# Performance work log

Measured on AMD Instinct MI355X. Metric: run time of the kernel, lower is better.

The kernel has to match this reference:

```python
import jax, jax.numpy as jnp
import numpy as np
import math

B, F, S, D, NH, L, DFF, M = 8, 48, 64, 512, 8, 4, 2048, 64
PERIOD = 30
NEG = -1e9
EPS = 1e-5

def _slopes(n):
    start = 2.0 ** (-2.0 ** -(math.log2(n) - 3))
    return np.array([start * (start ** i) for i in range(n)], dtype=np.float32)

def _biased_mask():  # (NH, F, F): causal mask + periodic ALiBi bias, alibi[i,j] = -((i-j)//period)
    i = np.arange(F)[:, None]; j = np.arange(F)[None, :]
    alibi = -((i - j) // PERIOD).astype(np.float32)
    return jnp.asarray(np.where(j <= i, _slopes(NH)[:, None, None] * alibi, NEG).astype(np.float32))

def _ppe():  # (F, D): periodic sinusoidal positional encoding (period 30)
    pos = np.arange(PERIOD, dtype=np.float32)[:, None]
    div = np.exp(np.arange(0, D, 2, dtype=np.float32) * (-math.log(10000.0) / D))
    pe = np.zeros((PERIOD, D), np.float32)
    pe[:, 0::2] = np.sin(pos * div)
    pe[:, 1::2] = np.cos(pos * div)
    return jnp.asarray(np.tile(pe, (F // PERIOD + 1, 1))[:F])

BIASED_MASK = _biased_mask()
PE = _ppe()
MEM_MASK = jnp.where(jnp.eye(F, dtype=bool), 0.0, NEG)  # enc_dec diagonal mask (frame i <-> content i)

def _ln(x, g, b):
    mu = x.mean(-1, keepdims=True)
    var = ((x - mu) ** 2).mean(-1, keepdims=True)
    return (x - mu) * jax.lax.rsqrt(var + EPS) * g + b

def _mha(q, k, v, in_w, in_b, out_w, out_b, nh, mask=None):
    Bq, Tq, d = q.shape
    Tk = k.shape[1]
    dh = d // nh
    wq, wk, wv = jnp.split(in_w, 3, axis=0)
    bq, bk, bv = jnp.split(in_b, 3, axis=0)
    qh = (q @ wq.T + bq).reshape(Bq, Tq, nh, dh).transpose(0, 2, 1, 3)
    kh = (k @ wk.T + bk).reshape(Bq, Tk, nh, dh).transpose(0, 2, 1, 3)
    vh = (v @ wv.T + bv).reshape(Bq, Tk, nh, dh).transpose(0, 2, 1, 3)
    s = jnp.einsum('bhqd,bhkd->bhqk', qh, kh) / jnp.sqrt(jnp.float32(dh))
    if mask is not None:
        s = s + mask
    o = jnp.einsum('bhqk,bhkd->bhqd', jax.nn.softmax(s, axis=-1), vh)
    return o.transpose(0, 2, 1, 3).reshape(Bq, Tq, d) @ out_w.T + out_b

def setup_inputs():
    key = jax.random.key(0)
    ks = iter(jax.random.split(key, 40))
    r = lambda *sh: jax.random.normal(next(ks), sh, jnp.float32) * 0.02
    return dict(
        content_code=jax.random.normal(next(ks), (B, F, D), jnp.float32),
        style_code=jax.random.normal(next(ks), (B, D), jnp.float32),
        style_hiddens=jax.random.normal(next(ks), (B, S, D), jnp.float32),
        init_state=jax.random.normal(next(ks), (B, M), jnp.float32),
        ca_in_w=r(3 * D, D), ca_in_b=r(3 * D), ca_out_w=r(D, D), ca_out_b=r(D),
        se_w=r(D, 2 * D), se_b=r(D),
        mm_w=r(D, M), mm_b=r(D),
        mmr_w=r(M, D), mmr_b=r(M),
        sa_in_w=r(L, 3 * D, D), sa_in_b=r(L, 3 * D), sa_out_w=r(L, D, D), sa_out_b=r(L, D),
        xa_in_w=r(L, 3 * D, D), xa_in_b=r(L, 3 * D), xa_out_w=r(L, D, D), xa_out_b=r(L, D),
        ff1_w=r(L, DFF, D), ff1_b=r(L, DFF), ff2_w=r(L, D, DFF), ff2_b=r(L, D),
        ln_g=jnp.ones((L, 3, D), jnp.float32), ln_b=jnp.zeros((L, 3, D), jnp.float32),
    )

def _forward(content_code, style_code, style_hiddens, init_state,
             ca_in_w, ca_in_b, ca_out_w, ca_out_b, se_w, se_b,
             mm_w, mm_b, mmr_w, mmr_b,
             sa_in_w, sa_in_b, sa_out_w, sa_out_b,
             xa_in_w, xa_in_b, xa_out_w, xa_out_b,
             ff1_w, ff1_b, ff2_w, ff2_b, ln_g, ln_b):
    style_emb_g = style_code[:, None, :]
    # 1-head cross-attn of each content frame against style hiddens; the torch code
    # computes this one query (frame) at a time, which is mathematically identical.
    sel = _mha(content_code, style_hiddens, style_hiddens,
               ca_in_w, ca_in_b, ca_out_w, ca_out_b, 1)  # (B, F, D)

    def emb_new(feat, i):  # style_emb_map(cat([feat, style_emb_l_i])) + global style
        return (jnp.concatenate([feat, sel[:, i:i + 1]], -1) @ se_w.T + se_b) + style_emb_g

    def decoder(x, mem):  # post-norm TransformerDecoder, relu FFN, eval (no dropout)
        T = x.shape[1]
        tgt = BIASED_MASK[None, :, :T, :T]
        mmask = MEM_MASK[:T][None, None]  # (1,1,T,F)
        for l in range(L):
            x = _ln(x + _mha(x, x, x, sa_in_w[l], sa_in_b[l], sa_out_w[l], sa_out_b[l], NH, tgt),
                    ln_g[l, 0], ln_b[l, 0])
            x = _ln(x + _mha(x, mem, mem, xa_in_w[l], xa_in_b[l], xa_out_w[l], xa_out_b[l], NH, mmask),
                    ln_g[l, 1], ln_b[l, 1])
            h = jax.nn.relu(x @ ff1_w[l].T + ff1_b[l]) @ ff2_w[l].T + ff2_b[l]
            x = _ln(x + h, ln_g[l, 2], ln_b[l, 2])
        return x

    dec_emb = emb_new((init_state @ mm_w.T + mm_b)[:, None], 0)  # (B,1,D)
    dec_out = None
    for i in range(F):
        dec_input = dec_emb + PE[:dec_emb.shape[1]]
        dec_out = decoder(dec_input, content_code) @ mmr_w.T + mmr_b  # (B, i+1, M)
        new = dec_out[:, -1:] @ mm_w.T + mm_b
        dec_emb = jnp.concatenate([dec_emb, emb_new(new, i)], axis=1)
    return dec_out, sel

def reference(content_code, style_code, style_hiddens, init_state,
              ca_in_w, ca_in_b, ca_out_w, ca_out_b, se_w, se_b,
              mm_w, mm_b, mmr_w, mmr_b,
              sa_in_w, sa_in_b, sa_out_w, sa_out_b,
              xa_in_w, xa_in_b, xa_out_w, xa_out_b,
              ff1_w, ff1_b, ff2_w, ff2_b, ln_g, ln_b):
    return _forward(content_code, style_code, style_hiddens, init_state,
                    ca_in_w, ca_in_b, ca_out_w, ca_out_b, se_w, se_b,
                    mm_w, mm_b, mmr_w, mmr_b,
                    sa_in_w, sa_in_b, sa_out_w, sa_out_b,
                    xa_in_w, xa_in_b, xa_out_w, xa_out_b,
                    ff1_w, ff1_b, ff2_w, ff2_b, ln_g, ln_b)
```

## Files before the change

### kernel.cpp

```cpp
#include <hip/hip_runtime.h>
#include <hip/hip_fp16.h>


typedef _Float16 h2 __attribute__((ext_vector_type(2)));
__device__ inline h2 u2h(unsigned u){ union{unsigned u; h2 h;} c; c.u=u; return c.h; }
#if __has_builtin(__builtin_amdgcn_fdot2)
__device__ inline float FDOT2(h2 a, h2 b, float c){ return __builtin_amdgcn_fdot2(a, b, c, false); }
#else
__device__ inline float FDOT2(h2 a, h2 b, float c){
  return fmaf((float)a.y, (float)b.y, fmaf((float)a.x, (float)b.x, c));
}
#endif

__device__ inline float aload(const float* p){
  return __hip_atomic_load(p, __ATOMIC_RELAXED, __HIP_MEMORY_SCOPE_AGENT);
}
__device__ inline void astore(float* p, float v){
  __hip_atomic_store(p, v, __ATOMIC_RELAXED, __HIP_MEMORY_SCOPE_AGENT);
}
__device__ inline unsigned aloadu(const unsigned* p){
  return __hip_atomic_load(p, __ATOMIC_RELAXED, __HIP_MEMORY_SCOPE_AGENT);
}
__device__ inline void astoreu(unsigned* p, unsigned v){
  __hip_atomic_store(p, v, __ATOMIC_RELAXED, __HIP_MEMORY_SCOPE_AGENT);
}

#define FD4(w,x) do{ a0=FDOT2(u2h((w).x),u2h((x).x),a0); a1=FDOT2(u2h((w).y),u2h((x).y),a1); \
                     a2=FDOT2(u2h((w).z),u2h((x).z),a2); a3=FDOT2(u2h((w).w),u2h((x).w),a3);}while(0)

__device__ inline float dot128s(const ushort* wrow, const ushort* xh){
  const uint4* w4=(const uint4*)wrow; const uint4* x4=(const uint4*)xh;
  float a0=0.f,a1=0.f,a2=0.f,a3=0.f;
  #pragma unroll
  for(int i=0;i<16;++i){ uint4 w=w4[i], x=x4[i]; FD4(w,x); }
  return (a0+a1)+(a2+a3);
}
__device__ inline float dot128p(const uint4 (&pw)[16], const ushort* xh){
  const uint4* x4=(const uint4*)xh;
  float a0=0.f,a1=0.f,a2=0.f,a3=0.f;
  #pragma unroll
  for(int i=0;i<16;++i){ uint4 w=pw[i], x=x4[i]; FD4(w,x); }
  return (a0+a1)+(a2+a3);
}
__device__ inline float dot128p8(const uint4 (&pw)[8], const ushort* wrow, const ushort* xh){
  const uint4* w4=(const uint4*)wrow; const uint4* x4=(const uint4*)xh;
  float a0=0.f,a1=0.f,a2=0.f,a3=0.f;
  #pragma unroll
  for(int i=0;i<8;++i){ uint4 w=pw[i], x=x4[i]; FD4(w,x); }
  #pragma unroll
  for(int i=8;i<16;++i){ uint4 w=w4[i], x=x4[i]; FD4(w,x); }
  return (a0+a1)+(a2+a3);
}
__device__ inline float dot32s(const ushort* wrow, const ushort* xh){
  const uint4* w4=(const uint4*)wrow; const uint4* x4=(const uint4*)xh;
  float a0=0.f,a1=0.f,a2=0.f,a3=0.f;
  #pragma unroll
  for(int i=0;i<4;++i){ uint4 w=w4[i], x=x4[i]; FD4(w,x); }
  return (a0+a1)+(a2+a3);
}
__device__ inline float dot_f32(const float* wrow, const float* x, int n){
  const float4* w4 = (const float4*)wrow;
  float a0=0.f,a1=0.f,a2=0.f,a3=0.f;
  #pragma unroll 4
  for (int i=0; i<(n>>2); ++i){
    float4 w = w4[i]; const float* xp = x + i*4;
    a0 = fmaf(w.x, xp[0], a0); a1 = fmaf(w.y, xp[1], a1);
    a2 = fmaf(w.z, xp[2], a2); a3 = fmaf(w.w, xp[3], a3);
  }
  return (a0+a1)+(a2+a3);
}
__device__ inline float dot64f_p8(const float4 (&pw)[8], const float* wrow, const float* x){
  const float4* w4=(const float4*)wrow;
  float a0=0.f,a1=0.f,a2=0.f,a3=0.f;
  #pragma unroll
  for(int i=0;i<8;++i){ float4 w=pw[i]; const float* xp=x+i*4;
    a0=fmaf(w.x,xp[0],a0); a1=fmaf(w.y,xp[1],a1); a2=fmaf(w.z,xp[2],a2); a3=fmaf(w.w,xp[3],a3);}
  #pragma unroll
  for(int i=8;i<16;++i){ float4 w=w4[i]; const float* xp=x+i*4;
    a0=fmaf(w.x,xp[0],a0); a1=fmaf(w.y,xp[1],a1); a2=fmaf(w.z,xp[2],a2); a3=fmaf(w.w,xp[3],a3);}
  return (a0+a1)+(a2+a3);
}

#define XSP(e) (((e)>>6)*68 + ((e)&63))
#define XHP(e) (((e)>>7)*136 + ((e)&127))

__global__ void k_transpose(const float* __restrict__ src, float* __restrict__ dst, int R, int C,
                            size_t sStr, size_t dStr){
  __shared__ float tile[32][33];
  int z = blockIdx.z;
  src += (size_t)z*sStr; dst += (size_t)z*dStr;
  int cb = blockIdx.x*32, rb = blockIdx.y*32;
  int tx = threadIdx.x, ty = threadIdx.y;
  for (int i=ty; i<32; i+=8) tile[i][tx] = src[(size_t)(rb+i)*C + cb+tx];
  __syncthreads();
  for (int i=ty; i<32; i+=8) dst[(size_t)(cb+i)*R + rb+tx] = tile[tx][i];
}

__global__ void k_castall(const float* __restrict__ s1, const float* __restrict__ s2,
                          const float* __restrict__ s3, const float* __restrict__ s4,
                          __half* __restrict__ d){
  const int N1=4*1536*512, N2=4*512*512, N3=4*2048*512, N4=4*512*2048;
  const int total = N1+N2+N3+N4;
  for (int i = blockIdx.x*256 + threadIdx.x; i < total; i += gridDim.x*256){
    float v;
    if (i < N1) v = s1[i];
    else if (i < N1+N2) v = s2[i-N1];
    else if (i < N1+N2+N3) v = s3[i-N1-N2];
    else v = s4[i-N1-N2-N3];
    d[i] = __float2half(v);
  }
}

__global__ void k_linear(const float* __restrict__ A, int lda,
                         const float* __restrict__ Wt, int ldw,
                         const float* __restrict__ bias,
                         float* __restrict__ C, int ldc,
                         int O, int Din,
                         size_t aStr, size_t wStr, size_t bStr, size_t cStr){
  __shared__ float xs[8*1024];
  __shared__ float red[4096];
  int tid = threadIdx.x;
  int r0 = blockIdx.y*8;
  int z = blockIdx.z;
  const float* Az = A + (size_t)z*aStr;
  const float* Wz = Wt + (size_t)z*wStr;
  const float* Bz = bias ? bias + (size_t)z*bStr : nullptr;
  float* Cz = C + (size_t)z*cStr;
  for (int idx=tid; idx<8*Din; idx+=256){
    int ri = idx / Din, d = idx - ri*Din;
    xs[idx] = Az[(size_t)(r0+ri)*lda + d];
  }
  __syncthreads();
  int op = tid & 63, kp = tid >> 6;
  int o = blockIdx.x*128 + op*2;
  int dq = Din >> 2;
  float a0[8] = {0,0,0,0,0,0,0,0}, a1[8] = {0,0,0,0,0,0,0,0};
  for (int d = kp*dq; d < kp*dq+dq; ++d){
    float2 w = *reinterpret_cast<const float2*>(&Wz[(size_t)d*ldw + o]);
    #pragma unroll
    for (int ri=0; ri<8; ++ri){ float x = xs[ri*Din+d]; a0[ri] += x*w.x; a1[ri] += x*w.y; }
  }
  #pragma unroll
  for (int ri=0; ri<8; ++ri){
    red[((kp*64+op)*8+ri)*2]   = a0[ri];
    red[((kp*64+op)*8+ri)*2+1] = a1[ri];
  }
  __syncthreads();
  for (int idx = tid; idx < 1024; idx += 256){
    int ri = idx >> 7, oc = idx & 127;
    int opp = oc >> 1, c = oc & 1;
    float v = red[((0*64+opp)*8+ri)*2 + c] + red[((1*64+opp)*8+ri)*2 + c]
            + red[((2*64+opp)*8+ri)*2 + c] + red[((3*64+opp)*8+ri)*2 + c];
    int oo = blockIdx.x*128 + oc;
    if (Bz) v += Bz[oo];
    Cz[(size_t)(r0+ri)*ldc + oo] = v;
  }
}

__global__ void k_pe(float* __restrict__ pe){
  int idx = blockIdx.x*256 + threadIdx.x;
  int t = idx >> 9, d = idx & 511;
  int p = t % 30;
  int i2 = d & ~1;
  float div = __expf(-(float)i2 * (9.210340371976184f/512.f));
  float ang = (float)p * div;
  pe[idx] = (d & 1) ? cosf(ang) : sinf(ang);
}

__global__ void k_sel_attn(const float* __restrict__ qh, const float* __restrict__ kh,
                           const float* __restrict__ vh, float* __restrict__ o){
  int bf = blockIdx.x;
  int b  = bf / 48;
  int tid = threadIdx.x;
  __shared__ float qs[512];
  __shared__ float ps[64];
  qs[tid] = qh[(size_t)bf*512 + tid];
  qs[tid+256] = qh[(size_t)bf*512 + tid + 256];
  __syncthreads();
  if (tid < 64){
    const float* kr = kh + (size_t)(b*64+tid)*512;
    float a = 0.f;
    for (int d=0; d<512; ++d) a += qs[d]*kr[d];
    ps[tid] = a * 0.04419417382415922f;
  }
  __syncthreads();
  if (tid == 0){
    float m = -1e30f;
    for (int j=0;j<64;++j) m = fmaxf(m, ps[j]);
    float s = 0.f;
    for (int j=0;j<64;++j){ float e = __expf(ps[j]-m); ps[j]=e; s+=e; }
    float iv = 1.f/s;
    for (int j=0;j<64;++j) ps[j] *= iv;
  }
  __syncthreads();
  float a0=0.f, a1=0.f;
  for (int j=0;j<64;++j){
    const float* vr = vh + (size_t)(b*64+j)*512;
    float pj = ps[j];
    a0 += pj*vr[tid]; a1 += pj*vr[tid+256];
  }
  o[(size_t)bf*512+tid] = a0;
  o[(size_t)bf*512+tid+256] = a1;
}

__global__ void k_cat_tail(const float* __restrict__ sel, float* __restrict__ cat){
  int idx = blockIdx.x*256 + threadIdx.x;
  int b = idx >> 9, d = idx & 511;
  cat[b*1024 + 512 + d] = sel[(size_t)(b*48)*512 + d];
}
__global__ void k_add_style(const float* __restrict__ embt, const float* __restrict__ style,
                            float* __restrict__ emb){
  int idx = blockIdx.x*256 + threadIdx.x;
  emb[idx] = embt[idx] + style[idx];
}

struct DP {
  unsigned* fl;
  float* z;
  float* emb;
  const ushort *Wqkv, *Wo, *Wf1, *Wf2;
  const float *xa_c, *pe;
  const float *sa_in_b, *sa_out_b, *ff1_b, *ff2_b;
  const float *mmr_w, *mmr_b, *mm_w, *mm_b, *se_w, *se_b;
  const float *ln_g, *ln_b, *style, *sel;
  float* dec_out;
};

__launch_bounds__(512, 2)
__global__ void k_decode(DP p){
  const int tid = threadIdx.x;
  const int i = blockIdx.x;
  const int role = ((i & 7) << 1) | ((i >> 3) & 1);
  const int b = i >> 4;
  const int h = role >> 1, half = role & 1;
  const float slope = exp2f(-(float)(h+1));

  __shared__ float kc[4*48*65];
  __shared__ float vs[4*48*64];
  __shared__ float xsp[8*68];
  __shared__ float red[512];
  __shared__ float qs[64], ps[64], d64[64];
  __shared__ float nsp[8*68];
  __shared__ float selp[8*68];
  __shared__ float lnred[16];
  __shared__ __align__(16) __half xhp[4*136];
  __shared__ __align__(16) __half anh[64];
  __shared__ __align__(16) __half hsh[128];

  unsigned* flb = p.fl + (size_t)b*48*9*16;
  float* zb = p.z + (size_t)b*48*8*512;

  auto waitz = [&](int tt, int ss, const float* src)->float{
    const unsigned* f = flb + (size_t)(tt*9+ss)*16;
    if (tid < 16){
      while (aloadu(f + tid) == 0u)
        __builtin_amdgcn_s_sleep(1);
    }
    __syncthreads();
    return aload(src + tid);
  };
  auto post = [&](int tt, int ss){
    __syncthreads();
    if (tid == 0)
      astoreu(flb + (size_t)(tt*9+ss)*16 + role, 1u);
  };
  auto lnorm = [&](float v, const float* g, const float* bb,
                   bool toXs, bool toXh)->float{
    float s = v, q = v*v;
    #pragma unroll
    for (int off=32; off>0; off>>=1){ s += __shfl_xor(s, off, 64); q += __shfl_xor(q, off, 64); }
    if ((tid & 63) == 0){ lnred[tid>>6] = s; lnred[8+(tid>>6)] = q; }
    __syncthreads();
    s = 0.f; q = 0.f;
    #pragma unroll
    for (int w=0; w<8; ++w){ s += lnred[w]; q += lnred[8+w]; }
    float mu = s * (1.f/512.f);
    float rs = rsqrtf(q*(1.f/512.f) - mu*mu + 1e-5f);
    float r = (v-mu)*rs*g[tid] + bb[tid];
    if (toXs) xsp[XSP(tid)] = r;
    if (toXh) xhp[XHP(tid)] = __float2half(r);
    __syncthreads();
    return r;
  };

  for (int t=0; t<48; ++t){
    for (int l=0; l<4; ++l){
      const float* xac = p.xa_c + ((size_t)l*384 + b*48 + t)*512;
      float xa = xac[tid];
      if (l == 3) selp[XSP(tid)] = p.sel[((size_t)b*48+t)*512 + tid];

      uint4 wq[16];
      const ushort* wqbase = nullptr;
      if (tid < 384){
        int row = tid >> 1, piece = tid & 1;
        int sec = row >> 6, dch = row & 63;
        int wrow = sec*512 + h*64 + dch;
        wqbase = p.Wqkv + ((size_t)l*1536 + wrow)*512 + piece*256;
        const uint4* w4 = (const uint4*)wqbase;
        #pragma unroll
        for (int k=0; k<16; ++k) wq[k] = w4[k];
      }

      if (l == 0){
        float pe0 = p.pe[t*512+tid];
        float e;
        if (t > 0) e = waitz(t-1, 8, p.emb + ((size_t)t*8+b)*512);
        else       e = aload(p.emb + ((size_t)t*8+b)*512 + tid);
        float x = e + pe0;
        xsp[XSP(tid)] = x; xhp[XHP(tid)] = __float2half(x);
        __syncthreads();
      } else {
        float z = waitz(t, (l-1)*2+1, zb + ((size_t)t*8 + (l-1)*2+1)*512);
        lnorm(z, p.ln_g + ((l-1)*3+2)*512, p.ln_b + ((l-1)*3+2)*512, true, true);
      }
      if (tid < 384){
        int row = tid >> 1, piece = tid & 1;
        int sec = row >> 6, dch = row & 63;
        int wrow = sec*512 + h*64 + dch;
        float acc = dot128p(wq, (const ushort*)(xhp + (2*piece)*136))
                  + dot128s((const ushort*)wqbase + 128,
                            (const ushort*)(xhp + (2*piece+1)*136));
        acc += __shfl_xor(acc, 1, 64);
        if (piece == 0){
          acc += p.sa_in_b[l*1536+wrow];
          if (sec == 0) qs[dch] = acc;
          else if (sec == 1) kc[(l*48+t)*65 + dch] = acc;
          else vs[(l*48+t)*64 + dch] = acc;
        }
      }
      __syncthreads();
      if (tid < 64){
        float sc = -1e30f;
        if (tid <= t){
          float a = 0.f;
          const float* kr = &kc[(l*48+tid)*65];
          #pragma unroll
          for (int d=0; d<64; ++d) a = fmaf(qs[d], kr[d], a);
          sc = a*0.125f - ((t-tid) >= 30 ? slope : 0.f);
        }
        float m = sc;
        #pragma unroll
        for (int off=32; off>0; off>>=1) m = fmaxf(m, __shfl_xor(m, off, 64));
        float e = (tid <= t) ? __expf(sc-m) : 0.f;
        float s = e;
        #pragma unroll
        for (int off=32; off>0; off>>=1) s += __shfl_xor(s, off, 64);
        ps[tid] = e / s;
      }
      __syncthreads();
      {
        int d = tid & 63, jq = tid >> 6;
        float a = 0.f;
        for (int j=jq*6; j<jq*6+6; ++j)
          if (j <= t) a = fmaf(ps[j], vs[(l*48+j)*64 + d], a);
        red[tid] = a;
      }
      __syncthreads();
      if (tid < 64){
        float a = red[tid]+red[64+tid]+red[128+tid]+red[192+tid]
                + red[256+tid]+red[320+tid]+red[384+tid]+red[448+tid];
        anh[tid] = __float2half(a);
      }
      __syncthreads();
      {
        int oi = tid >> 1, piece = tid & 1;
        int o = half*256 + oi;
        float acc = dot32s((const ushort*)(p.Wo + (((size_t)l*512+o)*512 + h*64) + piece*32),
                           (const ushort*)anh + piece*32);
        acc += __shfl_xor(acc, 1, 64);
        if (piece == 0){
          if (h == 0) acc += xsp[XSP(o)] + p.sa_out_b[l*512+o];
          unsafeAtomicAdd(zb + ((size_t)t*8 + l*2)*512 + o, acc);
        }
      }
      post(t, l*2);

      uint4 wf1[8], wf2[8];
      {
        int row = tid >> 2, piece = tid & 3;
        const uint4* w4 = (const uint4*)(p.Wf1 + ((size_t)l*2048 + role*128 + row)*512 + piece*128);
        #pragma unroll
        for (int k=0; k<8; ++k) wf1[k] = w4[k];
        const uint4* w42 = (const uint4*)(p.Wf2 + ((size_t)l*512 + tid)*2048 + role*128);
        #pragma unroll
        for (int k=0; k<8; ++k) wf2[k] = w42[k];
      }

      float r;
      {
        float z = waitz(t, l*2, zb + ((size_t)t*8 + l*2)*512);
        float w = lnorm(z, p.ln_g + (l*3)*512, p.ln_b + (l*3)*512, false, false);
        float u = w + xa;
        r = lnorm(u, p.ln_g + (l*3+1)*512, p.ln_b + (l*3+1)*512, false, true);
      }
      {
        int row = tid >> 2, piece = tid & 3;
        float a = dot128p8(wf1,
                           (const ushort*)(p.Wf1 + ((size_t)l*2048 + role*128 + row)*512 + piece*128),
                           (const ushort*)(xhp + piece*136));
        a += __shfl_xor(a, 1, 64);
        a += __shfl_xor(a, 2, 64);
        if (piece == 0)
          hsh[row] = __float2half(fmaxf(a + p.ff1_b[l*2048 + role*128 + row], 0.f));
      }
      __syncthreads();
      {
        float a0 = dot128p8(wf2,
                            (const ushort*)(p.Wf2 + ((size_t)l*512 + tid)*2048 + role*128),
                            (const ushort*)hsh);
        if (role == 0) a0 += r + p.ff2_b[l*512+tid];
        unsafeAtomicAdd(zb + ((size_t)t*8 + l*2+1)*512 + tid, a0);
      }
      post(t, l*2+1);
    }

    float4 wm[8];
    {
      int o8 = tid >> 3, p8 = tid & 7;
      const float4* w4 = (const float4*)(p.mmr_w + (size_t)o8*512 + p8*64);
      #pragma unroll
      for (int k=0; k<8; ++k) wm[k] = w4[k];
    }
    {
      float z = waitz(t, 7, zb + ((size_t)t*8 + 7)*512);
      lnorm(z, p.ln_g + 11*512, p.ln_b + 11*512, true, false);
    }
    {
      int o8 = tid >> 3, p8 = tid & 7;
      float a = dot64f_p8(wm, p.mmr_w + (size_t)o8*512 + p8*64, xsp + p8*68);
      a += __shfl_xor(a, 1, 64);
      a += __shfl_xor(a, 2, 64);
      a += __shfl_xor(a, 4, 64);
      if (p8 == 0) d64[o8] = a + p.mmr_b[o8];
    }
    __syncthreads();
    if (role == 0 && tid < 64) p.dec_out[((size_t)b*48+t)*64 + tid] = d64[tid];
    nsp[XSP(tid)] = dot_f32(p.mm_w + (size_t)tid*64, d64, 64) + p.mm_b[tid];
    __syncthreads();
    {
      int o5 = tid >> 4, p16 = tid & 15;
      int o = role*32 + o5;
      const float* xsrc = (p16 < 8) ? (nsp + p16*68) : (selp + (p16-8)*68);
      float acc = dot_f32(p.se_w + (size_t)o*1024 + p16*64, xsrc, 64);
      acc += __shfl_xor(acc, 1, 64);
      acc += __shfl_xor(acc, 2, 64);
      acc += __shfl_xor(acc, 4, 64);
      acc += __shfl_xor(acc, 8, 64);
      if (p16 == 0){
        acc += p.se_b[o] + p.style[(size_t)b*512+o];
        astore(p.emb + ((size_t)(t+1)*8+b)*512 + o, acc);
      }
    }
    post(t, 8);
  }
}

extern "C" void kernel_launch(void* const* d_in, const int* in_sizes, int n_in,
                              void* d_out, int out_size, void* d_ws, size_t ws_size,
                              hipStream_t stream){
  (void)in_sizes; (void)n_in; (void)out_size; (void)ws_size;
  const float* content = (const float*)d_in[0];
  const float* style   = (const float*)d_in[1];
  const float* shid    = (const float*)d_in[2];
  const float* init_st = (const float*)d_in[3];
  const float* ca_in_w = (const float*)d_in[4];
  const float* ca_in_b = (const float*)d_in[5];
  const float* ca_out_w= (const float*)d_in[6];
  const float* ca_out_b= (const float*)d_in[7];
  const float* se_w    = (const float*)d_in[8];
  const float* se_b    = (const float*)d_in[9];
  const float* mm_w    = (const float*)d_in[10];
  const float* mm_b    = (const float*)d_in[11];
  const float* mmr_w   = (const float*)d_in[12];
  const float* mmr_b   = (const float*)d_in[13];
  const float* sa_in_w = (const float*)d_in[14];
  const float* sa_in_b = (const float*)d_in[15];
  const float* sa_out_w= (const float*)d_in[16];
  const float* sa_out_b= (const float*)d_in[17];
  const float* xa_in_w = (const float*)d_in[18];
  const float* xa_in_b = (const float*)d_in[19];
  const float* xa_out_w= (const float*)d_in[20];
  const float* xa_out_b= (const float*)d_in[21];
  const float* ff1_w   = (const float*)d_in[22];
  const float* ff1_b   = (const float*)d_in[23];
  const float* ff2_w   = (const float*)d_in[24];
  const float* ff2_b   = (const float*)d_in[25];
  const float* ln_g    = (const float*)d_in[26];
  const float* ln_b    = (const float*)d_in[27];

  float* out = (float*)d_out;
  float* dec_out = out;
  float* sel = out + 8*48*64;

  char* base = (char*)d_ws;
  size_t cur = 0;
  auto alloc = [&](size_t bytes)->char*{
    char* pt = base + cur;
    cur += (bytes + 255) & ~(size_t)255;
    return pt;
  };
  unsigned* fl  = (unsigned*)alloc((size_t)8*48*9*16*4);
  float* zacc   = (float*)alloc((size_t)8*48*8*512*4);
  float* emb    = (float*)alloc((size_t)49*8*512*4);
  size_t zero_span = cur;
  ushort* WqkvH = (ushort*)alloc((size_t)4*1536*512*2);
  ushort* WoH   = (ushort*)alloc((size_t)4*512*512*2);
  ushort* Wf1H  = (ushort*)alloc((size_t)4*2048*512*2);
  ushort* Wf2H  = (ushort*)alloc((size_t)4*512*2048*2);
  float* Wt_mm    = (float*)alloc((size_t)64*512*4);
  float* Wt_se    = (float*)alloc((size_t)1024*512*4);
  float* Wt_ca_in = (float*)alloc((size_t)512*1536*4);
  float* Wt_ca_out= (float*)alloc((size_t)512*512*4);
  float* Wt_xa_v  = (float*)alloc((size_t)4*512*512*4);
  float* Wt_xa_o  = (float*)alloc((size_t)4*512*512*4);
  float* xa_c  = (float*)alloc((size_t)4*384*512*4);
  float* pe    = (float*)alloc((size_t)48*512*4);
  float* qh    = (float*)alloc((size_t)384*512*4);
  float* khb   = (float*)alloc((size_t)512*512*4);
  float* vhb   = (float*)alloc((size_t)512*512*4);
  float* attno = (float*)alloc((size_t)384*512*4);
  float* xtmp4 = (float*)alloc((size_t)4*384*512*4);
  float* catb  = (float*)alloc((size_t)8*1024*4);
  float* embt  = (float*)alloc((size_t)8*512*4);
  (void)vhb;

  hipMemsetAsync(fl, 0, zero_span, stream);

  dim3 tb(32,8);
  k_castall<<<4096, 256, 0, stream>>>(sa_in_w, sa_out_w, ff1_w, ff2_w, (__half*)WqkvH);
  k_transpose<<<dim3(16,16,4), tb, 0, stream>>>(xa_in_w + (size_t)1024*512, Wt_xa_v, 512, 512,
                                                (size_t)1536*512, (size_t)512*512);
  k_transpose<<<dim3(16,16,4), tb, 0, stream>>>(xa_out_w, Wt_xa_o, 512, 512,
                                                (size_t)512*512, (size_t)512*512);
  k_transpose<<<dim3(16,48), tb, 0, stream>>>(ca_in_w,  Wt_ca_in, 1536, 512, 0, 0);
  k_transpose<<<dim3(16,16), tb, 0, stream>>>(ca_out_w, Wt_ca_out, 512, 512, 0, 0);
  k_transpose<<<dim3(32,16), tb, 0, stream>>>(se_w,  Wt_se, 512, 1024, 0, 0);
  k_transpose<<<dim3(2,16),  tb, 0, stream>>>(mm_w,  Wt_mm, 512, 64, 0, 0);

  k_pe<<<96, 256, 0, stream>>>(pe);

  k_linear<<<dim3(4,48), 256, 0, stream>>>(content, 512, Wt_ca_in, 1536, ca_in_b, qh, 512, 512, 512, 0,0,0,0);
  k_linear<<<dim3(4,64,2), 256, 0, stream>>>(shid, 512, Wt_ca_in + 512, 1536, ca_in_b + 512, khb, 512, 512, 512,
                                             0, 512, 512, (size_t)512*512);
  k_sel_attn<<<384, 256, 0, stream>>>(qh, khb, vhb, attno);
  k_linear<<<dim3(4,48), 256, 0, stream>>>(attno, 512, Wt_ca_out, 512, ca_out_b, sel, 512, 512, 512, 0,0,0,0);

  k_linear<<<dim3(4,48,4), 256, 0, stream>>>(content, 512, Wt_xa_v, 512, xa_in_b + 1024, xtmp4, 512, 512, 512,
                                             0, (size_t)512*512, 1536, (size_t)384*512);
  k_linear<<<dim3(4,48,4), 256, 0, stream>>>(xtmp4, 512, Wt_xa_o, 512, xa_out_b, xa_c, 512, 512, 512,
                                             (size_t)384*512, (size_t)512*512, 512, (size_t)384*512);

  k_linear<<<dim3(4,1), 256, 0, stream>>>(init_st, 64, Wt_mm, 512, mm_b, catb, 1024, 512, 64, 0,0,0,0);
  k_cat_tail<<<16, 256, 0, stream>>>(sel, catb);
  k_linear<<<dim3(4,1), 256, 0, stream>>>(catb, 1024, Wt_se, 512, se_b, embt, 512, 512, 1024, 0,0,0,0);
  k_add_style<<<16, 256, 0, stream>>>(embt, style, emb);

  DP p;
  p.fl = fl; p.z = zacc; p.emb = emb;
  p.Wqkv = WqkvH; p.Wo = WoH; p.Wf1 = Wf1H; p.Wf2 = Wf2H;
  p.xa_c = xa_c; p.pe = pe;
  p.sa_in_b = sa_in_b; p.sa_out_b = sa_out_b; p.ff1_b = ff1_b; p.ff2_b = ff2_b;
  p.mmr_w = mmr_w; p.mmr_b = mmr_b; p.mm_w = mm_w; p.mm_b = mm_b;
  p.se_w = se_w; p.se_b = se_b; p.ln_g = ln_g; p.ln_b = ln_b;
  p.style = style; p.sel = sel; p.dec_out = dec_out;

  k_decode<<<dim3(128), dim3(512), 0, stream>>>(p);
}
```

Measured before the change: 5.172 ms.

## Fuse setup kernels and switch decode flags to counter-based sync

Merges the positional-encoding kernel into the weight cast kernel. Folds the selection-attention output projection into the attention kernel and computes the initial embedding in one kernel that reads untransposed weights, which removes several transposes and small launches. The decode kernel's per-role flag array becomes a single atomic counter per slot: one thread spins until it reaches 16 and producers increment it with fetch_add. The aim is less launch overhead and cheaper polling, at the cost of contended atomics and uncoalesced row-wise dot products in the fused kernels.

Result: no change. 5.103 ms (-1.3%).

```diff
diff --git a/kernel.cpp b/kernel.cpp
--- a/kernel.cpp
+++ b/kernel.cpp
@@ -16,12 +16,6 @@
   return __hip_atomic_load(p, __ATOMIC_RELAXED, __HIP_MEMORY_SCOPE_AGENT);
 }
 __device__ inline void astore(float* p, float v){
-  __hip_atomic_store(p, v, __ATOMIC_RELAXED, __HIP_MEMORY_SCOPE_AGENT);
-}
-__device__ inline unsigned aloadu(const unsigned* p){
-  return __hip_atomic_load(p, __ATOMIC_RELAXED, __HIP_MEMORY_SCOPE_AGENT);
-}
-__device__ inline void astoreu(unsigned* p, unsigned v){
   __hip_atomic_store(p, v, __ATOMIC_RELAXED, __HIP_MEMORY_SCOPE_AGENT);
 }
 
@@ -96,18 +90,29 @@
   for (int i=ty; i<32; i+=8) dst[(size_t)(cb+i)*R + rb+tx] = tile[tx][i];
 }
 
-__global__ void k_castall(const float* __restrict__ s1, const float* __restrict__ s2,
-                          const float* __restrict__ s3, const float* __restrict__ s4,
-                          __half* __restrict__ d){
+__global__ void k_castpe(const float* __restrict__ s1, const float* __restrict__ s2,
+                         const float* __restrict__ s3, const float* __restrict__ s4,
+                         __half* __restrict__ d, float* __restrict__ pe){
   const int N1=4*1536*512, N2=4*512*512, N3=4*2048*512, N4=4*512*2048;
-  const int total = N1+N2+N3+N4;
+  const int NW = N1+N2+N3+N4;
+  const int total = NW + 48*512;
   for (int i = blockIdx.x*256 + threadIdx.x; i < total; i += gridDim.x*256){
-    float v;
-    if (i < N1) v = s1[i];
-    else if (i < N1+N2) v = s2[i-N1];
-    else if (i < N1+N2+N3) v = s3[i-N1-N2];
-    else v = s4[i-N1-N2-N3];
-    d[i] = __float2half(v);
+    if (i < NW){
+      float v;
+      if (i < N1) v = s1[i];
+      else if (i < N1+N2) v = s2[i-N1];
+      else if (i < N1+N2+N3) v = s3[i-N1-N2];
+      else v = s4[i-N1-N2-N3];
+      d[i] = __float2half(v);
+    } else {
+      int idx = i - NW;
+      int t = idx >> 9, dd = idx & 511;
+      int p = t % 30;
+      int i2 = dd & ~1;
+      float div = __expf(-(float)i2 * (9.210340371976184f/512.f));
+      float ang = (float)p * div;
+      pe[idx] = (dd & 1) ? cosf(ang) : sinf(ang);
+    }
   }
 }
 
@@ -157,23 +162,16 @@
   }
 }
 
-__global__ void k_pe(float* __restrict__ pe){
-  int idx = blockIdx.x*256 + threadIdx.x;
-  int t = idx >> 9, d = idx & 511;
-  int p = t % 30;
-  int i2 = d & ~1;
-  float div = __expf(-(float)i2 * (9.210340371976184f/512.f));
-  float ang = (float)p * div;
-  pe[idx] = (d & 1) ? cosf(ang) : sinf(ang);
-}
-
-__global__ void k_sel_attn(const float* __restrict__ qh, const float* __restrict__ kh,
-                           const float* __restrict__ vh, float* __restrict__ o){
+__global__ void k_sel_attn_out(const float* __restrict__ qh, const float* __restrict__ kh,
+                               const float* __restrict__ vh,
+                               const float* __restrict__ ow, const float* __restrict__ ob,
+                               float* __restrict__ sel){
   int bf = blockIdx.x;
   int b  = bf / 48;
   int tid = threadIdx.x;
   __shared__ float qs[512];
   __shared__ float ps[64];
+  __shared__ float ao[512];
   qs[tid] = qh[(size_t)bf*512 + tid];
   qs[tid+256] = qh[(size_t)bf*512 + tid + 256];
   __syncthreads();
@@ -193,25 +191,41 @@
     for (int j=0;j<64;++j) ps[j] *= iv;
   }
   __syncthreads();
-  float a0=0.f, a1=0.f;
-  for (int j=0;j<64;++j){
-    const float* vr = vh + (size_t)(b*64+j)*512;
-    float pj = ps[j];
-    a0 += pj*vr[tid]; a1 += pj*vr[tid+256];
-  }
-  o[(size_t)bf*512+tid] = a0;
-  o[(size_t)bf*512+tid+256] = a1;
-}
-
-__global__ void k_cat_tail(const float* __restrict__ sel, float* __restrict__ cat){
-  int idx = blockIdx.x*256 + threadIdx.x;
-  int b = idx >> 9, d = idx & 511;
-  cat[b*1024 + 512 + d] = sel[(size_t)(b*48)*512 + d];
-}
-__global__ void k_add_style(const float* __restrict__ embt, const float* __restrict__ style,
-                            float* __restrict__ emb){
-  int idx = blockIdx.x*256 + threadIdx.x;
-  emb[idx] = embt[idx] + style[idx];
+  {
+    float a0=0.f, a1=0.f;
+    for (int j=0;j<64;++j){
+      const float* vr = vh + (size_t)(b*64+j)*512;
+      float pj = ps[j];
+      a0 += pj*vr[tid]; a1 += pj*vr[tid+256];
+    }
+    ao[tid] = a0; ao[tid+256] = a1;
+  }
+  __syncthreads();
+  {
+    float v0 = dot_f32(ow + (size_t)tid*512,       ao, 512) + ob[tid];
+    float v1 = dot_f32(ow + (size_t)(tid+256)*512, ao, 512) + ob[tid+256];
+    sel[(size_t)bf*512 + tid]       = v0;
+    sel[(size_t)bf*512 + tid + 256] = v1;
+  }
+}
+
+__global__ void k_emb0(const float* __restrict__ init_st,
+                       const float* __restrict__ mm_w, const float* __restrict__ mm_b,
+                       const float* __restrict__ sel,
+                       const float* __restrict__ se_w, const float* __restrict__ se_b,
+                       const float* __restrict__ style, float* __restrict__ emb){
+  int b = blockIdx.x;
+  int tid = threadIdx.x;
+  __shared__ float ini[64];
+  __shared__ float cat[1024];
+  if (tid < 64) ini[tid] = init_st[b*64 + tid];
+  cat[512 + tid] = sel[(size_t)(b*48)*512 + tid];
+  __syncthreads();
+  cat[tid] = dot_f32(mm_w + (size_t)tid*64, ini, 64) + mm_b[tid];
+  __syncthreads();
+  float v = dot_f32(se_w + (size_t)tid*1024, cat, 1024) + se_b[tid]
+          + style[(size_t)b*512 + tid];
+  emb[b*512 + tid] = v;
 }
 
 struct DP {
@@ -251,9 +265,9 @@
   float* zb = p.z + (size_t)b*48*8*512;
 
   auto waitz = [&](int tt, int ss, const float* src)->float{
-    const unsigned* f = flb + (size_t)(tt*9+ss)*16;
-    if (tid < 16){
-      while (aloadu(f + tid) == 0u)
+    const unsigned* c = flb + (size_t)(tt*9+ss)*16;
+    if (tid == 0){
+      while (__hip_atomic_load(c, __ATOMIC_RELAXED, __HIP_MEMORY_SCOPE_AGENT) < 16u)
         __builtin_amdgcn_s_sleep(1);
     }
     __syncthreads();
@@ -262,7 +276,8 @@
   auto post = [&](int tt, int ss){
     __syncthreads();
     if (tid == 0)
-      astoreu(flb + (size_t)(tt*9+ss)*16 + role, 1u);
+      __hip_atomic_fetch_add(flb + (size_t)(tt*9+ss)*16, 1u,
+                             __ATOMIC_RELAXED, __HIP_MEMORY_SCOPE_AGENT);
   };
   auto lnorm = [&](float v, const float* g, const float* bb,
                    bool toXs, bool toXh)->float{
@@ -507,10 +522,7 @@
   ushort* WoH   = (ushort*)alloc((size_t)4*512*512*2);
   ushort* Wf1H  = (ushort*)alloc((size_t)4*2048*512*2);
   ushort* Wf2H  = (ushort*)alloc((size_t)4*512*2048*2);
-  float* Wt_mm    = (float*)alloc((size_t)64*512*4);
-  float* Wt_se    = (float*)alloc((size_t)1024*512*4);
   float* Wt_ca_in = (float*)alloc((size_t)512*1536*4);
-  float* Wt_ca_out= (float*)alloc((size_t)512*512*4);
   float* Wt_xa_v  = (float*)alloc((size_t)4*512*512*4);
   float* Wt_xa_o  = (float*)alloc((size_t)4*512*512*4);
   float* xa_c  = (float*)alloc((size_t)4*384*512*4);
@@ -518,42 +530,30 @@
   float* qh    = (float*)alloc((size_t)384*512*4);
   float* khb   = (float*)alloc((size_t)512*512*4);
   float* vhb   = (float*)alloc((size_t)512*512*4);
-  float* attno = (float*)alloc((size_t)384*512*4);
   float* xtmp4 = (float*)alloc((size_t)4*384*512*4);
-  float* catb  = (float*)alloc((size_t)8*1024*4);
-  float* embt  = (float*)alloc((size_t)8*512*4);
   (void)vhb;
 
   hipMemsetAsync(fl, 0, zero_span, stream);
 
   dim3 tb(32,8);
-  k_castall<<<4096, 256, 0, stream>>>(sa_in_w, sa_out_w, ff1_w, ff2_w, (__half*)WqkvH);
+  k_castpe<<<4096, 256, 0, stream>>>(sa_in_w, sa_out_w, ff1_w, ff2_w, (__half*)WqkvH, pe);
   k_transpose<<<dim3(16,16,4), tb, 0, stream>>>(xa_in_w + (size_t)1024*512, Wt_xa_v, 512, 512,
                                                 (size_t)1536*512, (size_t)512*512);
   k_transpose<<<dim3(16,16,4), tb, 0, stream>>>(xa_out_w, Wt_xa_o, 512, 512,
                                                 (size_t)512*512, (size_t)512*512);
   k_transpose<<<dim3(16,48), tb, 0, stream>>>(ca_in_w,  Wt_ca_in, 1536, 512, 0, 0);
-  k_transpose<<<dim3(16,16), tb, 0, stream>>>(ca_out_w, Wt_ca_out, 512, 512, 0, 0);
-  k_transpose<<<dim3(32,16), tb, 0, stream>>>(se_w,  Wt_se, 512, 1024, 0, 0);
-  k_transpose<<<dim3(2,16),  tb, 0, stream>>>(mm_w,  Wt_mm, 512, 64, 0, 0);
-
-  k_pe<<<96, 256, 0, stream>>>(pe);
 
   k_linear<<<dim3(4,48), 256, 0, stream>>>(content, 512, Wt_ca_in, 1536, ca_in_b, qh, 512, 512, 512, 0,0,0,0);
   k_linear<<<dim3(4,64,2), 256, 0, stream>>>(shid, 512, Wt_ca_in + 512, 1536, ca_in_b + 512, khb, 512, 512, 512,
                                              0, 512, 512, (size_t)512*512);
-  k_sel_attn<<<384, 256, 0, stream>>>(qh, khb, vhb, attno);
-  k_linear<<<dim3(4,48), 256, 0, stream>>>(attno, 512, Wt_ca_out, 512, ca_out_b, sel, 512, 512, 512, 0,0,0,0);
+  k_sel_attn_out<<<384, 256, 0, stream>>>(qh, khb, vhb, ca_out_w, ca_out_b, sel);
 
   k_linear<<<dim3(4,48,4), 256, 0, stream>>>(content, 512, Wt_xa_v, 512, xa_in_b + 1024, xtmp4, 512, 512, 512,
                                              0, (size_t)512*512, 1536, (size_t)384*512);
   k_linear<<<dim3(4,48,4), 256, 0, stream>>>(xtmp4, 512, Wt_xa_o, 512, xa_out_b, xa_c, 512, 512, 512,
                                              (size_t)384*512, (size_t)512*512, 512, (size_t)384*512);
 
-  k_linear<<<dim3(4,1), 256, 0, stream>>>(init_st, 64, Wt_mm, 512, mm_b, catb, 1024, 512, 64, 0,0,0,0);
-  k_cat_tail<<<16, 256, 0, stream>>>(sel, catb);
-  k_linear<<<dim3(4,1), 256, 0, stream>>>(catb, 1024, Wt_se, 512, se_b, embt, 512, 512, 1024, 0,0,0,0);
-  k_add_style<<<16, 256, 0, stream>>>(embt, style, emb);
+  k_emb0<<<8, 512, 0, stream>>>(init_st, mm_w, mm_b, sel, se_w, se_b, style, emb);
 
   DP p;
   p.fl = fl; p.z = zacc; p.emb = emb;
```
